# Kernel optimization log

Hardware: AMD Instinct MI355X
Metric: run time of the kernel (lower is better)

The kernel has to match this reference:

```python
import jax, jax.numpy as jnp
import numpy as np

D_MODEL = 1024
NUM_HEADS = 16
HEAD_DIM = D_MODEL // NUM_HEADS
THETA = 10000.0


def _rope(x):
    # x: [B, H, S, Dk]; interleaved even/odd rotation as in the torch module
    *_, seq_len, d_k = x.shape
    d = d_k // 2
    inv_freq = 1.0 / (THETA ** (2.0 * jnp.arange(d, dtype=jnp.float32) / d_k))
    pos = jnp.arange(seq_len, dtype=jnp.float32)
    angles = pos[:, None] * inv_freq[None, :]  # [S, d]
    cos = jnp.cos(angles)
    sin = jnp.sin(angles)
    x_even = x[..., 0::2]
    x_odd = x[..., 1::2]
    rot_even = x_even * cos - x_odd * sin
    rot_odd = x_even * sin + x_odd * cos
    return jnp.stack([rot_even, rot_odd], axis=-1).reshape(x.shape)


def setup_inputs() -> dict:
    key = jax.random.key(0)
    ks = jax.random.split(key, 5)
    B, S = 4, 2048
    x = jax.random.normal(ks[0], (B, S, D_MODEL), dtype=jnp.float32)
    q_w = jax.random.uniform(ks[1], (D_MODEL, D_MODEL), dtype=jnp.float32)
    k_w = jax.random.uniform(ks[2], (D_MODEL, D_MODEL), dtype=jnp.float32)
    v_w = jax.random.uniform(ks[3], (D_MODEL, D_MODEL), dtype=jnp.float32)
    o_w = jax.random.uniform(ks[4], (D_MODEL, D_MODEL), dtype=jnp.float32)
    return {"x": x, "q_w": q_w, "k_w": k_w, "v_w": v_w, "o_w": o_w}


def reference(x, q_w, k_w, v_w, o_w):
    B, S, _ = x.shape
    def split_heads(t):
        return t.reshape(B, S, NUM_HEADS, HEAD_DIM).transpose(0, 2, 1, 3)  # [B,H,S,Dk]
    Q = split_heads(x @ q_w.T)
    K = split_heads(x @ k_w.T)
    V = split_heads(x @ v_w.T)
    Q = _rope(Q)
    K = _rope(K)
    scale = 1.0 / jnp.sqrt(jnp.float32(HEAD_DIM))
    scores = jnp.einsum('bhqd,bhkd->bhqk', Q, K) * scale  # [B,H,S,S]
    causal = jnp.tril(jnp.ones((S, S), dtype=bool))
    scores = jnp.where(causal[None, None], scores, -jnp.inf)
    attn = jax.nn.softmax(scores, axis=-1)
    out = jnp.einsum('bhqk,bhkd->bhqd', attn, V)  # [B,H,S,Dk]
    out = out.transpose(0, 2, 1, 3).reshape(B, S, D_MODEL)
    return out @ o_w.T
```

## Files before the change

kernel.cpp:

```cpp
#include <hip/hip_runtime.h>
#include <hip/hip_bf16.h>
#include <cstdint>
#include <cstddef>

#define D_MODEL   1024
#define NUM_HEADS 16
#define HEAD_DIM  64
#define SEQ       2048
#define BATCH     4
#define BH        (BATCH*NUM_HEADS)
#define MROWS     (BATCH*SEQ)

typedef _Float16 half8  __attribute__((ext_vector_type(8)));
typedef _Float16 half4v __attribute__((ext_vector_type(4)));
typedef float    floatx4 __attribute__((ext_vector_type(4)));

__device__ inline void gld_lds16(const void* g, void* l) {
    __builtin_amdgcn_global_load_lds(
        (__attribute__((address_space(1))) void*)g,
        (__attribute__((address_space(3))) void*)l,
        16, 0, 0);
}

__global__ void rope_table(float2* __restrict__ tab) {
    const int i = blockIdx.x * blockDim.x + threadIdx.x;
    const int p = i & 31, s = i >> 5;
    const double inv = pow(10000.0, -(double)p / 32.0);
    const double ang = (double)s * inv;
    tab[i] = make_float2((float)cos(ang), (float)sin(ang));
}

__global__ void f32_split_f16(const float* __restrict__ in,
                              _Float16* __restrict__ hi,
                              _Float16* __restrict__ lo, int n4) {
    int i = blockIdx.x * blockDim.x + threadIdx.x;
    if (i >= n4) return;
    float4 v = ((const float4*)in)[i];
    half4v h = { (_Float16)v.x, (_Float16)v.y, (_Float16)v.z, (_Float16)v.w };
    half4v l = { (_Float16)(v.x - (float)h.x), (_Float16)(v.y - (float)h.y),
                 (_Float16)(v.z - (float)h.z), (_Float16)(v.w - (float)h.w) };
    ((half4v*)hi)[i] = h;
    ((half4v*)lo)[i] = l;
}

__global__ void conv_weights(const float* __restrict__ qw, const float* __restrict__ kw,
                             const float* __restrict__ vw, const float* __restrict__ ow,
                             _Float16* __restrict__ qwh, _Float16* __restrict__ qwl,
                             _Float16* __restrict__ kwh, _Float16* __restrict__ kwl,
                             _Float16* __restrict__ vwh, _Float16* __restrict__ owh) {
    const int i = blockIdx.x * blockDim.x + threadIdx.x;
    const int which = i >> 18;
    const int j = i & 262143;
    const float4 v = ((const float4*)(which == 0 ? qw : which == 1 ? kw :
                                      which == 2 ? vw : ow))[j];
    half4v h = { (_Float16)v.x, (_Float16)v.y, (_Float16)v.z, (_Float16)v.w };
    if (which < 2) {
        half4v l = { (_Float16)(v.x - (float)h.x), (_Float16)(v.y - (float)h.y),
                     (_Float16)(v.z - (float)h.z), (_Float16)(v.w - (float)h.w) };
        ((half4v*)(which ? kwh : qwh))[j] = h;
        ((half4v*)(which ? kwl : qwl))[j] = l;
    } else {
        ((half4v*)(which == 2 ? vwh : owh))[j] = h;
    }
}

__global__ __launch_bounds__(256)
void gemm_bt(const _Float16* __restrict__ A, const _Float16* __restrict__ B,
             float* __restrict__ Cout, int M, int N, int K) {
    __shared__ _Float16 As[128*32];
    __shared__ _Float16 Bs[128*32];

    const int nb = N >> 7;
    const int bx = blockIdx.x % nb;
    const int by = blockIdx.x / nb;
    const int m0 = by << 7, n0 = bx << 7;

    const int t    = threadIdx.x;
    const int w    = t >> 6;
    const int lane = t & 63;
    const int r    = lane & 15;
    const int quad = lane >> 4;
    const int wm   = (w >> 1) << 6;
    const int wn   = (w & 1) << 6;

    const int srow = lane >> 2;
    const int scol = (lane & 3) << 3;

    floatx4 acc[4][4];
    #pragma unroll
    for (int i = 0; i < 4; i++)
        #pragma unroll
        for (int j = 0; j < 4; j++)
            acc[i][j] = (floatx4){0.f, 0.f, 0.f, 0.f};

    for (int k0 = 0; k0 < K; k0 += 32) {
        __syncthreads();
        #pragma unroll
        for (int p = 0; p < 2; ++p) {
            const int rbase = p*64 + w*16;
            gld_lds16(&A[(size_t)(m0 + rbase + srow)*K + k0 + scol], &As[rbase*32]);
            gld_lds16(&B[(size_t)(n0 + rbase + srow)*K + k0 + scol], &Bs[rbase*32]);
        }
        __syncthreads();

        half8 af[4], bf[4];
        #pragma unroll
        for (int i = 0; i < 4; i++)
            af[i] = *(const half8*)&As[(wm + i*16 + r)*32 + quad*8];
        #pragma unroll
        for (int j = 0; j < 4; j++)
            bf[j] = *(const half8*)&Bs[(wn + j*16 + r)*32 + quad*8];

        #pragma unroll
        for (int i = 0; i < 4; i++)
            #pragma unroll
            for (int j = 0; j < 4; j++)
                acc[i][j] = __builtin_amdgcn_mfma_f32_16x16x32_f16(
                                af[i], bf[j], acc[i][j], 0, 0, 0);
    }

    #pragma unroll
    for (int i = 0; i < 4; i++)
        #pragma unroll
        for (int j = 0; j < 4; j++)
            #pragma unroll
            for (int v = 0; v < 4; v++) {
                const int m = m0 + wm + i*16 + quad*4 + v;
                const int n = n0 + wn + j*16 + r;
                Cout[(size_t)m*N + n] = acc[i][j][v];
            }
}

__global__ __launch_bounds__(256)
void gemm_qkv(const _Float16* __restrict__ Axh, const _Float16* __restrict__ Axl,
              const _Float16* __restrict__ qwh, const _Float16* __restrict__ qwl,
              const _Float16* __restrict__ kwh, const _Float16* __restrict__ kwl,
              const _Float16* __restrict__ vwh,
              _Float16* __restrict__ Qhi, _Float16* __restrict__ Qlo,
              _Float16* __restrict__ Khi, _Float16* __restrict__ Klo,
              _Float16* __restrict__ Vt,  const float2* __restrict__ tab) {
    __shared__ _Float16 Ash[128*32];
    __shared__ _Float16 Asl[128*32];
    __shared__ _Float16 Bsh[128*32];
    __shared__ _Float16 Bsl[128*32];

    const int bxa = blockIdx.x;
    const int bx  = bxa % 24;
    const int by  = bxa / 24;
    const int wt  = bx >> 3;
    const int n0  = (bx & 7) << 7;
    const int m0  = by << 7;

    const _Float16* Bh = (wt == 0) ? qwh : (wt == 1) ? kwh : vwh;
    const _Float16* Bl = (wt == 0) ? qwl : kwl;

    const int t    = threadIdx.x;
    const int w    = t >> 6;
    const int lane = t & 63;
    const int r    = lane & 15;
    const int quad = lane >> 4;
    const int wm   = (w >> 1) << 6;
    const int wn   = (w & 1) << 6;

    const int srow = lane >> 2;
    const int scol = (lane & 3) << 3;

    floatx4 acc[4][4];
    #pragma unroll
    for (int i = 0; i < 4; i++)
        #pragma unroll
        for (int j = 0; j < 4; j++)
            acc[i][j] = (floatx4){0.f, 0.f, 0.f, 0.f};

    for (int k0 = 0; k0 < 1024; k0 += 32) {
        __syncthreads();
        #pragma unroll
        for (int p = 0; p < 2; ++p) {
            const int rbase = p*64 + w*16;
            const size_t ga = (size_t)(m0 + rbase + srow)*1024 + k0 + scol;
            const size_t gb = (size_t)(n0 + rbase + srow)*1024 + k0 + scol;
            gld_lds16(&Axh[ga], &Ash[rbase*32]);
            gld_lds16(&Bh [gb], &Bsh[rbase*32]);
            if (wt < 2) {
                gld_lds16(&Axl[ga], &Asl[rbase*32]);
                gld_lds16(&Bl [gb], &Bsl[rbase*32]);
            }
        }
        __syncthreads();

        half8 ah[4], bh[4];
        #pragma unroll
        for (int i = 0; i < 4; i++)
            ah[i] = *(const half8*)&Ash[(wm + i*16 + r)*32 + quad*8];
        #pragma unroll
        for (int j = 0; j < 4; j++)
            bh[j] = *(const half8*)&Bsh[(wn + j*16 + r)*32 + quad*8];

        if (wt < 2) {
            half8 al[4], bl[4];
            #pragma unroll
            for (int i = 0; i < 4; i++)
                al[i] = *(const half8*)&Asl[(wm + i*16 + r)*32 + quad*8];
            #pragma unroll
            for (int j = 0; j < 4; j++)
                bl[j] = *(const half8*)&Bsl[(wn + j*16 + r)*32 + quad*8];
            #pragma unroll
            for (int i = 0; i < 4; i++)
                #pragma unroll
                for (int j = 0; j < 4; j++) {
                    acc[i][j] = __builtin_amdgcn_mfma_f32_16x16x32_f16(
                                    ah[i], bh[j], acc[i][j], 0, 0, 0);
                    acc[i][j] = __builtin_amdgcn_mfma_f32_16x16x32_f16(
                                    ah[i], bl[j], acc[i][j], 0, 0, 0);
                    acc[i][j] = __builtin_amdgcn_mfma_f32_16x16x32_f16(
                                    al[i], bh[j], acc[i][j], 0, 0, 0);
                }
        } else {
            #pragma unroll
            for (int i = 0; i < 4; i++)
                #pragma unroll
                for (int j = 0; j < 4; j++)
                    acc[i][j] = __builtin_amdgcn_mfma_f32_16x16x32_f16(
                                    ah[i], bh[j], acc[i][j], 0, 0, 0);
        }
    }

    if (wt < 2) {
        _Float16* Chi = wt ? Khi : Qhi;
        _Float16* Clo = wt ? Klo : Qlo;
        #pragma unroll
        for (int i = 0; i < 4; i++) {
            #pragma unroll
            for (int v = 0; v < 4; v++) {
                const int m  = m0 + wm + i*16 + quad*4 + v;
                const int b  = m >> 11;
                const int s_ = m & 2047;
                #pragma unroll
                for (int j = 0; j < 4; j++) {
                    const int n = n0 + wn + j*16 + r;
                    const int h = n >> 6, d = n & 63;
                    const float val = acc[i][j][v];
                    const float pv  = __shfl_xor(val, 1);
                    const float2 cs = tab[s_*32 + (d >> 1)];
                    const float res = (r & 1) ? (pv*cs.y + val*cs.x)
                                              : (val*cs.x - pv*cs.y);
                    const size_t idx = ((((size_t)b*NUM_HEADS + h)*SEQ + s_) << 6) + d;
                    const _Float16 hv = (_Float16)res;
                    Chi[idx] = hv;
                    Clo[idx] = (_Float16)(res - (float)hv);
                }
            }
        }
    } else {
        #pragma unroll
        for (int i = 0; i < 4; i++) {
            #pragma unroll
            for (int v = 0; v < 4; v++) {
                const int m  = m0 + wm + i*16 + quad*4 + v;
                const int b  = m >> 11;
                const int s_ = m & 2047;
                #pragma unroll
                for (int j = 0; j < 4; j++) {
                    const int n = n0 + wn + j*16 + r;
                    const int h = n >> 6, d = n & 63;
                    Vt[((((size_t)b*NUM_HEADS + h)*HEAD_DIM + d) << 11) + s_]
                        = (_Float16)acc[i][j][v];
                }
            }
        }
    }
}

#define PSTR 72
__global__ __launch_bounds__(512)
void flash_attn(const _Float16* __restrict__ Qhi, const _Float16* __restrict__ Qlo,
                const _Float16* __restrict__ Khi, const _Float16* __restrict__ Klo,
                const _Float16* __restrict__ Vt,  _Float16* __restrict__ AO) {
    __shared__ _Float16 Ksh0[64*32];
    __shared__ _Float16 Ksh1[64*32];
    __shared__ _Float16 Ksl0[64*32];
    __shared__ _Float16 Ksl1[64*32];
    __shared__ _Float16 Vs0 [64*32];
    __shared__ _Float16 Vs1 [64*32];
    __shared__ _Float16 Pl  [8][16*PSTR];

    const int t    = threadIdx.x;
    const int w    = t >> 6;
    const int lane = t & 63;
    const int r    = lane & 15;
    const int quad = lane >> 4;

    const int bx = blockIdx.x;
    const int bh = bx & 63;
    const int qb = 15 - (bx >> 6);
    const int q0w = qb*128 + w*16;
    const int b  = bh >> 4, h = bh & 15;

    const _Float16* Qh_ = Qhi + (size_t)bh * SEQ * HEAD_DIM;
    const _Float16* Ql_ = Qlo + (size_t)bh * SEQ * HEAD_DIM;
    const _Float16* Khg = Khi + (size_t)bh * SEQ * HEAD_DIM;
    const _Float16* Klg = Klo + (size_t)bh * SEQ * HEAD_DIM;
    const _Float16* Vtg = Vt  + (size_t)bh * HEAD_DIM * SEQ;

    half8 qh[2], ql[2];
    #pragma unroll
    for (int c = 0; c < 2; ++c) {
        qh[c] = *(const half8*)&Qh_[(size_t)(q0w + r)*64 + c*32 + quad*8];
        ql[c] = *(const half8*)&Ql_[(size_t)(q0w + r)*64 + c*32 + quad*8];
    }

    floatx4 ot[4];
    #pragma unroll
    for (int dt = 0; dt < 4; ++dt) ot[dt] = (floatx4){0.f,0.f,0.f,0.f};
    float mi = -1e30f, li = 0.f;

    const int sr = lane >> 2;
    const int sc = (lane & 3) << 3;

    const int niter = 2*qb + 2;
    for (int kt = 0; kt < niter; ++kt) {
        const int k0 = kt << 6;

        __syncthreads();
        #pragma unroll
        for (int i = 0; i < 3; ++i) {
            const int strip = w + (i << 3);
            const int plane = strip >> 2;
            const int rb    = (strip & 3) << 4;
            const int row   = rb + sr;
            switch (plane) {
            case 0: gld_lds16(&Khg[(size_t)(k0 + row)*64 +      sc], &Ksh0[rb*32]); break;
            case 1: gld_lds16(&Khg[(size_t)(k0 + row)*64 + 32 + sc], &Ksh1[rb*32]); break;
            case 2: gld_lds16(&Klg[(size_t)(k0 + row)*64 +      sc], &Ksl0[rb*32]); break;
            case 3: gld_lds16(&Klg[(size_t)(k0 + row)*64 + 32 + sc], &Ksl1[rb*32]); break;
            case 4: gld_lds16(&Vtg[(size_t)row*SEQ + k0 +       sc], &Vs0 [rb*32]); break;
            case 5: gld_lds16(&Vtg[(size_t)row*SEQ + k0 + 32 +  sc], &Vs1 [rb*32]); break;
            }
        }
        __syncthreads();

        if (k0 > q0w + 15) continue;

        float s[16];
        #pragma unroll
        for (int sub = 0; sub < 4; ++sub) {
            floatx4 a = (floatx4){0.f,0.f,0.f,0.f};
            const int fr = (sub*16 + r)*32 + quad*8;
            const half8 kh0 = *(const half8*)&Ksh0[fr];
            const half8 kh1 = *(const half8*)&Ksh1[fr];
            const half8 kl0 = *(const half8*)&Ksl0[fr];
            const half8 kl1 = *(const half8*)&Ksl1[fr];
            a = __builtin_amdgcn_mfma_f32_16x16x32_f16(kh0, qh[0], a, 0, 0, 0);
            a = __builtin_amdgcn_mfma_f32_16x16x32_f16(kh1, qh[1], a, 0, 0, 0);
            a = __builtin_amdgcn_mfma_f32_16x16x32_f16(kh0, ql[0], a, 0, 0, 0);
            a = __builtin_amdgcn_mfma_f32_16x16x32_f16(kh1, ql[1], a, 0, 0, 0);
            a = __builtin_amdgcn_mfma_f32_16x16x32_f16(kl0, qh[0], a, 0, 0, 0);
            a = __builtin_amdgcn_mfma_f32_16x16x32_f16(kl1, qh[1], a, 0, 0, 0);
            #pragma unroll
            for (int v = 0; v < 4; ++v) s[sub*4 + v] = a[v] * 0.125f;
        }

        if (k0 + 63 > q0w) {
            #pragma unroll
            for (int sub = 0; sub < 4; ++sub)
                #pragma unroll
                for (int v = 0; v < 4; ++v)
                    if (k0 + sub*16 + quad*4 + v > q0w + r)
                        s[sub*4 + v] = -1e30f;
        }

        float tm = s[0];
        #pragma unroll
        for (int i = 1; i < 16; ++i) tm = fmaxf(tm, s[i]);
        tm = fmaxf(tm, __shfl_xor(tm, 16));
        tm = fmaxf(tm, __shfl_xor(tm, 32));
        const float mn = fmaxf(mi, tm);
        const float alpha = __expf(mi - mn);
        mi = mn;
        float rs = 0.f;
        #pragma unroll
        for (int i = 0; i < 16; ++i) { s[i] = __expf(s[i] - mn); rs += s[i]; }
        rs += __shfl_xor(rs, 16);
        rs += __shfl_xor(rs, 32);
        li = li*alpha + rs;
        #pragma unroll
        for (int dt = 0; dt < 4; ++dt)
            #pragma unroll
            for (int v = 0; v < 4; ++v) ot[dt][v] *= alpha;

        #pragma unroll
        for (int sub = 0; sub < 4; ++sub) {
            half4v pk = { (_Float16)s[sub*4+0], (_Float16)s[sub*4+1],
                          (_Float16)s[sub*4+2], (_Float16)s[sub*4+3] };
            *(half4v*)&Pl[w][r*PSTR + sub*16 + quad*4] = pk;
        }

        #pragma unroll
        for (int c = 0; c < 2; ++c) {
            const half8 pf = *(const half8*)&Pl[w][r*PSTR + c*32 + quad*8];
            const _Float16* Vsc = c ? Vs1 : Vs0;
            #pragma unroll
            for (int dt = 0; dt < 4; ++dt) {
                const half8 vf = *(const half8*)&Vsc[(dt*16 + r)*32 + quad*8];
                ot[dt] = __builtin_amdgcn_mfma_f32_16x16x32_f16(vf, pf, ot[dt], 0, 0, 0);
            }
        }
    }

    const float inv = 1.0f / li;
    const int q = q0w + r;
    #pragma unroll
    for (int dt = 0; dt < 4; ++dt) {
        half4v o = { (_Float16)(ot[dt][0]*inv), (_Float16)(ot[dt][1]*inv),
                     (_Float16)(ot[dt][2]*inv), (_Float16)(ot[dt][3]*inv) };
        *(half4v*)&AO[((size_t)(b*SEQ + q))*D_MODEL + h*HEAD_DIM + dt*16 + quad*4] = o;
    }
}

extern "C" void kernel_launch(void* const* d_in, const int* in_sizes, int n_in,
                              void* d_out, int out_size, void* d_ws, size_t ws_size,
                              hipStream_t stream) {
    const float* x  = (const float*)d_in[0];
    const float* qw = (const float*)d_in[1];
    const float* kw = (const float*)d_in[2];
    const float* vw = (const float*)d_in[3];
    const float* ow = (const float*)d_in[4];
    float* out = (float*)d_out;

    _Float16* xh  = (_Float16*)d_ws;
    _Float16* xl  = xh  + (size_t)MROWS * D_MODEL;
    _Float16* qwh = xl  + (size_t)MROWS * D_MODEL;
    _Float16* qwl = qwh + (size_t)D_MODEL * D_MODEL;
    _Float16* kwh = qwl + (size_t)D_MODEL * D_MODEL;
    _Float16* kwl = kwh + (size_t)D_MODEL * D_MODEL;
    _Float16* vwh = kwl + (size_t)D_MODEL * D_MODEL;
    _Float16* owh = vwh + (size_t)D_MODEL * D_MODEL;
    _Float16* Qhi = owh + (size_t)D_MODEL * D_MODEL;
    _Float16* Qlo = Qhi + (size_t)MROWS * D_MODEL;
    _Float16* Khi = Qlo + (size_t)MROWS * D_MODEL;
    _Float16* Klo = Khi + (size_t)MROWS * D_MODEL;
    _Float16* Vt  = Klo + (size_t)MROWS * D_MODEL;
    _Float16* AO  = Vt  + (size_t)MROWS * D_MODEL;
    float2*   tab = (float2*)(AO + (size_t)MROWS * D_MODEL);

    rope_table<<<(SEQ*32)/256, 256, 0, stream>>>(tab);

    const int nx4 = MROWS * D_MODEL / 4;
    f32_split_f16<<<nx4/256, 256, 0, stream>>>(x, xh, xl, nx4);
    conv_weights<<<(4*262144)/256, 256, 0, stream>>>(qw, kw, vw, ow,
                                                     qwh, qwl, kwh, kwl, vwh, owh);

    gemm_qkv<<<64*24, 256, 0, stream>>>(xh, xl, qwh, qwl, kwh, kwl, vwh,
                                        Qhi, Qlo, Khi, Klo, Vt, tab);

    flash_attn<<<BH * (SEQ/128), 512, 0, stream>>>(Qhi, Qlo, Khi, Klo, Vt, AO);

    gemm_bt<<<(MROWS/128)*(D_MODEL/128), 256, 0, stream>>>(AO, owh, out,
                                                           MROWS, D_MODEL, D_MODEL);
}
```

Measured before the change: 394.0 us.

## Stage QKV epilogue through LDS for vector stores; shrink attention blocks to 64 queries

The QKV GEMM epilogue now writes accumulators into shared memory and reads them back row-wise, so RoPE is applied on contiguous even/odd pairs and Q/K/V are written with 16-byte vector stores instead of scattered scalar stores. This mainly helps the transposed V output, which was previously written with badly strided 2-byte stores. Flash attention switches from 128-query blocks of 8 waves to 64-query blocks of 4 waves. Each wave now does useful work on every loaded KV tile, which removes the skipped-iteration waste and causal imbalance, at the cost of more blocks and more repeated K/V loads.

```diff
diff --git a/kernel.cpp b/kernel.cpp
--- a/kernel.cpp
+++ b/kernel.cpp
@@ -139,10 +139,11 @@
               _Float16* __restrict__ Qhi, _Float16* __restrict__ Qlo,
               _Float16* __restrict__ Khi, _Float16* __restrict__ Klo,
               _Float16* __restrict__ Vt,  const float2* __restrict__ tab) {
-    __shared__ _Float16 Ash[128*32];
-    __shared__ _Float16 Asl[128*32];
-    __shared__ _Float16 Bsh[128*32];
-    __shared__ _Float16 Bsl[128*32];
+    __shared__ _Float16 smem[4*4096];
+    _Float16* Ash = smem;
+    _Float16* Asl = smem + 4096;
+    _Float16* Bsh = smem + 8192;
+    _Float16* Bsl = smem + 12288;
 
     const int bxa = blockIdx.x;
     const int bx  = bxa % 24;
@@ -225,54 +226,73 @@
         }
     }
 
+    __syncthreads();
+    float* sc = (float*)smem + w*1088;
+    const int g  = lane & 7;
+    const int rw = lane >> 3;
+    const int hh = (n0 + wn) >> 6;
+
     if (wt < 2) {
         _Float16* Chi = wt ? Khi : Qhi;
         _Float16* Clo = wt ? Klo : Qlo;
         #pragma unroll
         for (int i = 0; i < 4; i++) {
             #pragma unroll
-            for (int v = 0; v < 4; v++) {
-                const int m  = m0 + wm + i*16 + quad*4 + v;
-                const int b  = m >> 11;
-                const int s_ = m & 2047;
-                #pragma unroll
-                for (int j = 0; j < 4; j++) {
-                    const int n = n0 + wn + j*16 + r;
-                    const int h = n >> 6, d = n & 63;
-                    const float val = acc[i][j][v];
-                    const float pv  = __shfl_xor(val, 1);
-                    const float2 cs = tab[s_*32 + (d >> 1)];
-                    const float res = (r & 1) ? (pv*cs.y + val*cs.x)
-                                              : (val*cs.x - pv*cs.y);
-                    const size_t idx = ((((size_t)b*NUM_HEADS + h)*SEQ + s_) << 6) + d;
-                    const _Float16 hv = (_Float16)res;
-                    Chi[idx] = hv;
-                    Clo[idx] = (_Float16)(res - (float)hv);
+            for (int j = 0; j < 4; j++)
+                #pragma unroll
+                for (int v = 0; v < 4; v++)
+                    sc[(quad*4 + v)*68 + j*16 + r] = acc[i][j][v];
+            #pragma unroll
+            for (int rg = 0; rg < 2; rg++) {
+                const int row = rw + rg*8;
+                const int m   = m0 + wm + i*16 + row;
+                const int bb  = m >> 11, s_ = m & 2047;
+                const float4 va = *(const float4*)&sc[row*68 + g*8];
+                const float4 vb = *(const float4*)&sc[row*68 + g*8 + 4];
+                const float vv[8] = {va.x, va.y, va.z, va.w,
+                                     vb.x, vb.y, vb.z, vb.w};
+                half8 hv, lv;
+                #pragma unroll
+                for (int p2 = 0; p2 < 4; p2++) {
+                    const float2 cs = tab[s_*32 + g*4 + p2];
+                    const float e0 = vv[2*p2], o0 = vv[2*p2+1];
+                    const float re = e0*cs.x - o0*cs.y;
+                    const float ro = e0*cs.y + o0*cs.x;
+                    const _Float16 rh = (_Float16)re;
+                    const _Float16 oh = (_Float16)ro;
+                    hv[2*p2]   = rh; lv[2*p2]   = (_Float16)(re - (float)rh);
+                    hv[2*p2+1] = oh; lv[2*p2+1] = (_Float16)(ro - (float)oh);
                 }
+                const size_t idx = ((((size_t)bb*NUM_HEADS + hh)*SEQ + s_) << 6) + g*8;
+                *(half8*)&Chi[idx] = hv;
+                *(half8*)&Clo[idx] = lv;
             }
         }
     } else {
+        const int d = lane;
         #pragma unroll
         for (int i = 0; i < 4; i++) {
             #pragma unroll
-            for (int v = 0; v < 4; v++) {
-                const int m  = m0 + wm + i*16 + quad*4 + v;
-                const int b  = m >> 11;
-                const int s_ = m & 2047;
-                #pragma unroll
-                for (int j = 0; j < 4; j++) {
-                    const int n = n0 + wn + j*16 + r;
-                    const int h = n >> 6, d = n & 63;
-                    Vt[((((size_t)b*NUM_HEADS + h)*HEAD_DIM + d) << 11) + s_]
-                        = (_Float16)acc[i][j][v];
-                }
+            for (int j = 0; j < 4; j++)
+                #pragma unroll
+                for (int v = 0; v < 4; v++)
+                    sc[(quad*4 + v)*68 + j*16 + r] = acc[i][j][v];
+            #pragma unroll
+            for (int rg = 0; rg < 2; rg++) {
+                const int m  = m0 + wm + i*16 + rg*8;
+                const int bb = m >> 11, s_ = m & 2047;
+                half8 ov;
+                #pragma unroll
+                for (int rr = 0; rr < 8; rr++)
+                    ov[rr] = (_Float16)sc[(rg*8 + rr)*68 + d];
+                *(half8*)&Vt[((((size_t)bb*NUM_HEADS + hh)*HEAD_DIM + d) << 11) + s_] = ov;
             }
         }
     }
 }
 
 #define PSTR 72
-__global__ __launch_bounds__(512)
+__global__ __launch_bounds__(256)
 void flash_attn(const _Float16* __restrict__ Qhi, const _Float16* __restrict__ Qlo,
                 const _Float16* __restrict__ Khi, const _Float16* __restrict__ Klo,
                 const _Float16* __restrict__ Vt,  _Float16* __restrict__ AO) {
@@ -282,7 +302,7 @@
     __shared__ _Float16 Ksl1[64*32];
     __shared__ _Float16 Vs0 [64*32];
     __shared__ _Float16 Vs1 [64*32];
-    __shared__ _Float16 Pl  [8][16*PSTR];
+    __shared__ _Float16 Pl  [4][16*PSTR];
 
     const int t    = threadIdx.x;
     const int w    = t >> 6;
@@ -292,8 +312,8 @@
 
     const int bx = blockIdx.x;
     const int bh = bx & 63;
-    const int qb = 15 - (bx >> 6);
-    const int q0w = qb*128 + w*16;
+    const int qb = 31 - (bx >> 6);
+    const int q0w = qb*64 + w*16;
     const int b  = bh >> 4, h = bh & 15;
 
     const _Float16* Qh_ = Qhi + (size_t)bh * SEQ * HEAD_DIM;
@@ -317,29 +337,24 @@
     const int sr = lane >> 2;
     const int sc = (lane & 3) << 3;
 
-    const int niter = 2*qb + 2;
+    const int niter = qb + 1;
     for (int kt = 0; kt < niter; ++kt) {
         const int k0 = kt << 6;
 
         __syncthreads();
-        #pragma unroll
-        for (int i = 0; i < 3; ++i) {
-            const int strip = w + (i << 3);
-            const int plane = strip >> 2;
-            const int rb    = (strip & 3) << 4;
-            const int row   = rb + sr;
-            switch (plane) {
-            case 0: gld_lds16(&Khg[(size_t)(k0 + row)*64 +      sc], &Ksh0[rb*32]); break;
-            case 1: gld_lds16(&Khg[(size_t)(k0 + row)*64 + 32 + sc], &Ksh1[rb*32]); break;
-            case 2: gld_lds16(&Klg[(size_t)(k0 + row)*64 +      sc], &Ksl0[rb*32]); break;
-            case 3: gld_lds16(&Klg[(size_t)(k0 + row)*64 + 32 + sc], &Ksl1[rb*32]); break;
-            case 4: gld_lds16(&Vtg[(size_t)row*SEQ + k0 +       sc], &Vs0 [rb*32]); break;
-            case 5: gld_lds16(&Vtg[(size_t)row*SEQ + k0 + 32 +  sc], &Vs1 [rb*32]); break;
-            }
-        }
-        __syncthreads();
-
-        if (k0 > q0w + 15) continue;
+        {
+            const int rb  = w << 4;
+            const int row = rb + sr;
+            const size_t kr = (size_t)(k0 + row)*64;
+            gld_lds16(&Khg[kr +      sc], &Ksh0[rb*32]);
+            gld_lds16(&Khg[kr + 32 + sc], &Ksh1[rb*32]);
+            gld_lds16(&Klg[kr +      sc], &Ksl0[rb*32]);
+            gld_lds16(&Klg[kr + 32 + sc], &Ksl1[rb*32]);
+            const size_t vr = (size_t)row*SEQ + k0;
+            gld_lds16(&Vtg[vr +      sc], &Vs0[rb*32]);
+            gld_lds16(&Vtg[vr + 32 + sc], &Vs1[rb*32]);
+        }
+        __syncthreads();
 
         float s[16];
         #pragma unroll
@@ -360,7 +375,7 @@
             for (int v = 0; v < 4; ++v) s[sub*4 + v] = a[v] * 0.125f;
         }
 
-        if (k0 + 63 > q0w) {
+        if (kt == niter - 1) {
             #pragma unroll
             for (int sub = 0; sub < 4; ++sub)
                 #pragma unroll
@@ -453,7 +468,7 @@
     gemm_qkv<<<64*24, 256, 0, stream>>>(xh, xl, qwh, qwl, kwh, kwl, vwh,
                                         Qhi, Qlo, Khi, Klo, Vt, tab);
 
-    flash_attn<<<BH * (SEQ/128), 512, 0, stream>>>(Qhi, Qlo, Khi, Klo, Vt, AO);
+    flash_attn<<<BH * (SEQ/64), 256, 0, stream>>>(Qhi, Qlo, Khi, Klo, Vt, AO);
 
     gemm_bt<<<(MROWS/128)*(D_MODEL/128), 256, 0, stream>>>(AO, owh, out,
                                                            MROWS, D_MODEL, D_MODEL);
```

Measured after the change: 379.0 us. 3.8% less time.
